# Kernel tuning notes

Hardware: AMD Instinct MI355X
Metric: run time of the kernel (lower is better)

The kernel has to match this reference:

```python
import jax, jax.numpy as jnp
import numpy as np

DRN = 0.4
TWO_PI = 2.0 * np.pi


def _mlp(x, ws, bs):
    # torch_geometric MLP with act='LeakyRelu' (slope 0.01), dropout=0 (eval), norm treated as identity (eval running stats)
    for w, b in zip(ws[:-1], bs[:-1]):
        x = jax.nn.leaky_relu(x @ w + b, 0.01)
    return x @ ws[-1] + bs[-1]


def _conv(x, ws, bs):
    # x: [B, N, F] = [pt, h..., ang_re, ang_im]. Dense masked equivalent of radius-graph EdgeConv.
    ang = x[..., -2:]
    d2 = jnp.sum((ang[:, :, None, :] - ang[:, None, :, :]) ** 2, -1)
    adj = (d2 <= DRN * DRN).astype(x.dtype)  # [B,N,N], i=target, j=source, self-loops included (radius ball)
    h = x[..., 1:-2]
    B, N, H = h.shape
    hi = jnp.broadcast_to(h[:, :, None, :], (B, N, N, H))
    hj = jnp.broadcast_to(h[:, None, :, :], (B, N, N, H))
    re, im = ang[..., 0], ang[..., 1]
    r2 = re * re + im * im
    nrm = jnp.maximum(jnp.sqrt(r2[:, :, None] * r2[:, None, :]), 1e-12)
    cos = (re[:, :, None] * re[:, None, :] + im[:, :, None] * im[:, None, :]) / nrm
    sin = (im[:, :, None] * re[:, None, :] - re[:, :, None] * im[:, None, :]) / nrm
    feat = jnp.concatenate([hi, hj, hj - hi, cos[..., None], sin[..., None]], -1)
    m = _mlp(feat, ws, bs)  # [B,N,N,H_out+1]
    # pt-weighted aggregation: message pt is the TARGET's pt (x_i[:, :1] in torch code)
    pt = x[..., 0]
    msg_pt = pt[:, :, None] * adj
    denom = jnp.sum(msg_pt, -1, keepdims=True)
    w = jnp.where(denom > 0, msg_pt / denom, 0.0)  # nan_to_num equivalent
    agg = jnp.einsum('bij,bijk->bik', w, m)
    sw = jnp.sum(w, -1)
    agg_pt = pt * sw                      # sum_j w * pt_i
    agg_ang = ang * sw[..., None]          # sum_j w * ang_i
    # phase renormalization: exp(2*pi*i*gamma) * (re + i*im)
    gamma = agg[..., -1]
    c, s = jnp.cos(TWO_PI * gamma), jnp.sin(TWO_PI * gamma)
    re2 = c * agg_ang[..., 0] - s * agg_ang[..., 1]
    im2 = s * agg_ang[..., 0] + c * agg_ang[..., 1]
    return jnp.concatenate([agg_pt[..., None], agg[..., :-1], re2[..., None], im2[..., None]], -1)


def _forward(pt, angles, c0w, c0b, c1w, c1b, rw, rb):
    absz = jnp.sqrt(jnp.sum(angles ** 2, -1))  # |view_as_complex(angles)|
    x = jnp.concatenate([pt[..., None], absz[..., None], angles], -1)
    x = _conv(x, c0w, c0b)
    x = _conv(x, c1w, c1b)
    # pt-weighted readout over particles
    ptf = x[..., 0]
    denom = jnp.sum(ptf, -1, keepdims=True)
    wj = jnp.where(denom > 0, ptf / denom, 0.0)
    xg = jnp.einsum('bn,bnf->bf', wj, x[..., 1:])
    logits = _mlp(xg[:, :-2], rw, rb)
    return jnp.concatenate([jax.nn.sigmoid(logits), xg[:, -2:]], -1)


def setup_inputs() -> dict:
    key = jax.random.key(0)
    ks = jax.random.split(key, 16)
    B, N = 128, 128
    pt = jax.random.uniform(ks[0], (B, N), jnp.float32, 0.05, 1.0)  # all > 0 so mask is all-true
    angles = 0.25 * jax.random.normal(ks[1], (B, N, 2), jnp.float32)

    def lin(k, i, o):
        return (0.2 / np.sqrt(i)) * jax.random.normal(k, (i, o), jnp.float32) * np.sqrt(i)

    H = 16
    return {
        'pt': pt, 'angles': angles,
        'c0_w0': lin(ks[2], 5, H), 'c0_b0': jnp.zeros((H,), jnp.float32),
        'c0_w1': lin(ks[3], H, H + 1), 'c0_b1': jnp.zeros((H + 1,), jnp.float32),
        'c1_w0': lin(ks[4], 3 * H + 2, H), 'c1_b0': jnp.zeros((H,), jnp.float32),
        'c1_w1': lin(ks[5], H, H + 1), 'c1_b1': jnp.zeros((H + 1,), jnp.float32),
        'r_w0': lin(ks[6], H, 32), 'r_b0': jnp.zeros((32,), jnp.float32),
        'r_w1': lin(ks[7], 32, 32), 'r_b1': jnp.zeros((32,), jnp.float32),
        'r_w2': lin(ks[8], 32, 1), 'r_b2': jnp.zeros((1,), jnp.float32),
    }


def reference(pt, angles, c0_w0, c0_b0, c0_w1, c0_b1, c1_w0, c1_b0, c1_w1, c1_b1, r_w0, r_b0, r_w1, r_b1, r_w2, r_b2):
    return _forward(pt, angles, (c0_w0, c0_w1), (c0_b0, c0_b1), (c1_w0, c1_w1), (c1_b0, c1_b1), (r_w0, r_w1, r_w2), (r_b0, r_b1, r_b2))
```

## Files before the change

### kernel.cpp

```cpp
#include <hip/hip_runtime.h>
#include <math.h>


#define BB 128
#define NN 128
#define BN (BB * NN)
#define TWO_PI_F 6.283185307179586f

template <int CTRL>
__device__ __forceinline__ float dpp_add(float x) {
    int t = __builtin_amdgcn_update_dpp(0, __float_as_int(x), CTRL, 0xF, 0xF, true);
    return x + __int_as_float(t);
}

__device__ __forceinline__ float wave_sum64(float x) {
    x = dpp_add<0xB1>(x);
    x = dpp_add<0x4E>(x);
    x = dpp_add<0x114>(x);
    x = dpp_add<0x118>(x);
    x = dpp_add<0x142>(x);
    x = dpp_add<0x143>(x);
    return __int_as_float(__builtin_amdgcn_readlane(__float_as_int(x), 63));
}

template <int L>
__global__ __launch_bounds__(256) void conv_kernel(
    const float* __restrict__ ang,
    const float* __restrict__ u,
    const float* __restrict__ v,
    const float* __restrict__ w0,
    const float* __restrict__ b0,
    const float* __restrict__ w1,
    const float* __restrict__ b1,
    const float* __restrict__ nw0,
    const float* __restrict__ nb0,
    float* __restrict__ out_u,
    float* __restrict__ out_v,
    float* __restrict__ out_ang,
    float* __restrict__ y)
{
    const int lane = threadIdx.x & 63;
    const int wid  = threadIdx.x >> 6;
    const int ni   = __builtin_amdgcn_readfirstlane(blockIdx.x * 4 + wid);
    const int base = ni & ~(NN - 1);

    const float rei = ang[2 * ni], imi = ang[2 * ni + 1];
    const float r2i = rei * rei + imi * imi;

    constexpr int cosrow = (L == 0) ? 3 : 48;

    float u0b[16];
    float q0[16];
    if constexpr (L == 0) {
        float abszi = __builtin_amdgcn_sqrtf(r2i);
        #pragma unroll
        for (int k = 0; k < 16; ++k) {
            u0b[k] = fmaf(abszi, w0[k] - w0[32 + k], b0[k]);
            q0[k]  = w0[16 + k] + w0[32 + k];
        }
    } else {
        #pragma unroll
        for (int k = 0; k < 16; ++k) u0b[k] = u[ni * 16 + k];
    }

    float A[16];
    #pragma unroll
    for (int k = 0; k < 16; ++k) A[k] = 0.0f;
    int deg = 0;

    #pragma unroll
    for (int jj = 0; jj < 2; ++jj) {
        const int nj = base + lane + jj * 64;
        const float rej = ang[2 * nj], imj = ang[2 * nj + 1];

        const float dre = rei - rej, dim = imi - imj;
        const float d2 = dre * dre + dim * dim;
        const bool isadj = (d2 <= 0.16f);
        deg += (int)__popcll(__ballot(isadj));
        const float adjf = isadj ? 1.0f : 0.0f;

        const float r2j = rej * rej + imj * imj;
        const float inv = fminf(rsqrtf(r2i * r2j), 1e12f);
        const float cosv = fmaf(rei, rej, imi * imj) * inv;
        const float sinv = fmaf(imi, rej, -(rei * imj)) * inv;

        float abszj = 0.0f;
        float vj[16];
        if constexpr (L == 0) {
            abszj = __builtin_amdgcn_sqrtf(r2j);
        } else {
            const float4* vp = (const float4*)(v + (size_t)nj * 16);
            float4 a0 = vp[0], a1 = vp[1], a2 = vp[2], a3 = vp[3];
            vj[0] = a0.x; vj[1] = a0.y; vj[2]  = a0.z; vj[3]  = a0.w;
            vj[4] = a1.x; vj[5] = a1.y; vj[6]  = a1.z; vj[7]  = a1.w;
            vj[8] = a2.x; vj[9] = a2.y; vj[10] = a2.z; vj[11] = a2.w;
            vj[12] = a3.x; vj[13] = a3.y; vj[14] = a3.z; vj[15] = a3.w;
        }

        #pragma unroll
        for (int k = 0; k < 16; ++k) {
            float z;
            if constexpr (L == 0) z = fmaf(abszj, q0[k], u0b[k]);
            else                  z = u0b[k] + vj[k];
            z = fmaf(cosv, w0[cosrow * 16 + k], z);
            z = fmaf(sinv, w0[(cosrow + 1) * 16 + k], z);
            float a = fmaxf(z, 0.01f * z);
            A[k] = fmaf(a, adjf, A[k]);
        }
    }

    float Ak[16];
    #pragma unroll
    for (int k = 0; k < 16; ++k) Ak[k] = wave_sum64(A[k]);
    const float invdeg = 1.0f / (float)deg;

    float aggv = 0.0f;
    if (lane < 17) {
        float s = 0.0f;
        #pragma unroll
        for (int k = 0; k < 16; ++k) s = fmaf(Ak[k], w1[k * 17 + lane], s);
        aggv = fmaf(s, invdeg, b1[lane]);
    }

    __shared__ float h1s[4][16];

    if constexpr (L == 0) {
        if (lane < 16) h1s[wid][lane] = aggv;
        if (lane == 16) {
            float th = TWO_PI_F * aggv;
            float cs = cosf(th), sn = sinf(th);
            out_ang[2 * ni]     = cs * rei - sn * imi;
            out_ang[2 * ni + 1] = sn * rei + cs * imi;
        }
        __syncthreads();
        if (lane < 32) {
            const int k = lane & 15;
            const bool isU = lane < 16;
            const int off = isU ? 0 : 256;
            const float sgn = isU ? -1.0f : 1.0f;
            float acc = isU ? nb0[k] : 0.0f;
            #pragma unroll
            for (int c = 0; c < 16; ++c) {
                float wa  = nw0[off + c * 16 + k];
                float wcv = nw0[512 + c * 16 + k];
                acc = fmaf(h1s[wid][c], fmaf(sgn, wcv, wa), acc);
            }
            if (isU) out_u[ni * 16 + k] = acc;
            else     out_v[ni * 16 + k] = acc;
        }
    } else {
        if (lane < 16) y[ni * 18 + lane] = aggv;
        if (lane == 16) {
            float th = TWO_PI_F * aggv;
            float cs = cosf(th), sn = sinf(th);
            y[ni * 18 + 16] = cs * rei - sn * imi;
            y[ni * 18 + 17] = sn * rei + cs * imi;
        }
    }
}

__global__ __launch_bounds__(128) void readout_kernel(
    const float* __restrict__ pt,
    const float* __restrict__ y,
    const float* __restrict__ w0, const float* __restrict__ b0,
    const float* __restrict__ w1, const float* __restrict__ b1,
    const float* __restrict__ w2, const float* __restrict__ b2,
    float* __restrict__ out) {
    int b = blockIdx.x;
    int tid = threadIdx.x;
    int n = b * NN + tid;
    float ptf = pt[n];
    const float* yn = y + (size_t)n * 18;

    __shared__ float sred[2][18];
    __shared__ float xg[18];
    __shared__ float h1s[32];

    float tot = ptf;
#pragma unroll
    for (int off = 32; off; off >>= 1) tot += __shfl_xor(tot, off);
    if ((tid & 63) == 0) sred[tid >> 6][0] = tot;
    __syncthreads();
    float denom = sred[0][0] + sred[1][0];
    float wj = (denom > 0.0f) ? (ptf / denom) : 0.0f;
    __syncthreads();

    float vals[18];
#pragma unroll
    for (int f = 0; f < 18; ++f) vals[f] = wj * yn[f];
#pragma unroll
    for (int f = 0; f < 18; ++f) {
        float s = vals[f];
#pragma unroll
        for (int off = 32; off; off >>= 1) s += __shfl_xor(s, off);
        vals[f] = s;
    }
    if ((tid & 63) == 0) {
#pragma unroll
        for (int f = 0; f < 18; ++f) sred[tid >> 6][f] = vals[f];
    }
    __syncthreads();
    if (tid < 18) xg[tid] = sred[0][tid] + sred[1][tid];
    __syncthreads();

    if (tid < 32) {
        float h = b0[tid];
#pragma unroll
        for (int k = 0; k < 16; ++k) h = fmaf(xg[k], w0[k * 32 + tid], h);
        h = (h >= 0.0f) ? h : 0.01f * h;
        h1s[tid] = h;
    }
    __syncthreads();
    if (tid < 32) {
        float h = b1[tid];
#pragma unroll
        for (int k = 0; k < 32; ++k) h = fmaf(h1s[k], w1[k * 32 + tid], h);
        h = (h >= 0.0f) ? h : 0.01f * h;
        float p = h * w2[tid];
#pragma unroll
        for (int off = 16; off; off >>= 1) p += __shfl_xor(p, off, 32);
        if (tid == 0) {
            float logit = p + b2[0];
            out[b * 3 + 0] = 1.0f / (1.0f + expf(-logit));
            out[b * 3 + 1] = xg[16];
            out[b * 3 + 2] = xg[17];
        }
    }
}

extern "C" void kernel_launch(void* const* d_in, const int* in_sizes, int n_in,
                              void* d_out, int out_size, void* d_ws, size_t ws_size,
                              hipStream_t stream) {
    const float* pt    = (const float*)d_in[0];
    const float* ang   = (const float*)d_in[1];
    const float* c0_w0 = (const float*)d_in[2];
    const float* c0_b0 = (const float*)d_in[3];
    const float* c0_w1 = (const float*)d_in[4];
    const float* c0_b1 = (const float*)d_in[5];
    const float* c1_w0 = (const float*)d_in[6];
    const float* c1_b0 = (const float*)d_in[7];
    const float* c1_w1 = (const float*)d_in[8];
    const float* c1_b1 = (const float*)d_in[9];
    const float* r_w0  = (const float*)d_in[10];
    const float* r_b0  = (const float*)d_in[11];
    const float* r_w1  = (const float*)d_in[12];
    const float* r_b1  = (const float*)d_in[13];
    const float* r_w2  = (const float*)d_in[14];
    const float* r_b2  = (const float*)d_in[15];
    float* out = (float*)d_out;
    float* ws = (float*)d_ws;

    float* u1b  = ws;
    float* v1   = u1b + (size_t)BN * 16;
    float* ang1 = v1 + (size_t)BN * 16;
    float* y1   = ang1 + (size_t)BN * 2;

    hipLaunchKernelGGL((conv_kernel<0>), dim3(BN / 4), dim3(256), 0, stream,
                       ang, (const float*)nullptr, (const float*)nullptr,
                       c0_w0, c0_b0, c0_w1, c0_b1,
                       c1_w0, c1_b0, u1b, v1, ang1, (float*)nullptr);
    hipLaunchKernelGGL((conv_kernel<1>), dim3(BN / 4), dim3(256), 0, stream,
                       ang1, u1b, v1,
                       c1_w0, (const float*)nullptr, c1_w1, c1_b1,
                       (const float*)nullptr, (const float*)nullptr,
                       (float*)nullptr, (float*)nullptr, (float*)nullptr, y1);
    hipLaunchKernelGGL(readout_kernel, dim3(BB), dim3(128), 0, stream,
                       pt, y1, r_w0, r_b0, r_w1, r_b1, r_w2, r_b2, out);
}
```

Before: 37.12 us.

## Remap conv kernels to one lane per target node and fuse readout pooling

Each lane now owns one target node, and the 128 source nodes are split across the four waves of a block. Source angles and features are staged once in LDS, and per-wave partial sums are combined through shared memory. This replaces the earlier design of one wave per target node with 16 cross-lane DPP reductions per node, and cuts the grid from 4096 blocks to 256. The pt-weighted pooling moves into conv1 as per-block partial sums, so the y buffer disappears and the readout kernel shrinks to a tiny MLP. In exchange the grid has only 256 blocks of four waves, so occupancy is low and the per-lane serial work is longer; the 1e12 clamp on the inverse norm is also dropped.

```diff
diff --git a/kernel.cpp b/kernel.cpp
--- a/kernel.cpp
+++ b/kernel.cpp
@@ -5,7 +5,6 @@
 #define BB 128
 #define NN 128
 #define BN (BB * NN)
-#define TWO_PI_F 6.283185307179586f
 
 template <int CTRL>
 __device__ __forceinline__ float dpp_add(float x) {
@@ -23,205 +22,304 @@
     return __int_as_float(__builtin_amdgcn_readlane(__float_as_int(x), 63));
 }
 
-template <int L>
-__global__ __launch_bounds__(256) void conv_kernel(
+__global__ __launch_bounds__(256) void conv0_kernel(
     const float* __restrict__ ang,
-    const float* __restrict__ u,
-    const float* __restrict__ v,
     const float* __restrict__ w0,
     const float* __restrict__ b0,
     const float* __restrict__ w1,
     const float* __restrict__ b1,
     const float* __restrict__ nw0,
     const float* __restrict__ nb0,
-    float* __restrict__ out_u,
-    float* __restrict__ out_v,
-    float* __restrict__ out_ang,
-    float* __restrict__ y)
+    float* __restrict__ ang1,
+    float* __restrict__ u1,
+    float* __restrict__ v1)
 {
-    const int lane = threadIdx.x & 63;
-    const int wid  = threadIdx.x >> 6;
-    const int ni   = __builtin_amdgcn_readfirstlane(blockIdx.x * 4 + wid);
-    const int base = ni & ~(NN - 1);
-
-    const float rei = ang[2 * ni], imi = ang[2 * ni + 1];
-    const float r2i = rei * rei + imi * imi;
-
-    constexpr int cosrow = (L == 0) ? 3 : 48;
-
-    float u0b[16];
-    float q0[16];
-    if constexpr (L == 0) {
-        float abszi = __builtin_amdgcn_sqrtf(r2i);
+    const int tid  = threadIdx.x;
+    const int lane = tid & 63;
+    const int wid  = tid >> 6;
+    const int b     = blockIdx.x >> 1;
+    const int ihalf = blockIdx.x & 1;
+    const int nodebase = b * NN;
+    const int ni = nodebase + ihalf * 64 + lane;
+
+    __shared__ float4 jdat[NN];
+    __shared__ float Ap[4][17][64];
+
+    if (tid < NN) {
+        float2 a = ((const float2*)ang)[nodebase + tid];
+        float r2 = a.x * a.x + a.y * a.y;
+        float absz = __builtin_amdgcn_sqrtf(r2);
+        float inv = __builtin_amdgcn_rsqf(r2);
+        jdat[tid] = make_float4(a.x, a.y, absz, inv);
+    }
+    __syncthreads();
+
+    const float4 my = jdat[ihalf * 64 + lane];
+    const float rei = my.x, imi = my.y, abszi = my.z, invi = my.w;
+
+    float u0b[16], q0[16];
+    #pragma unroll
+    for (int k = 0; k < 16; ++k) {
+        u0b[k] = fmaf(abszi, w0[k] - w0[32 + k], b0[k]);
+        q0[k]  = w0[16 + k] + w0[32 + k];
+    }
+
+    float A[16];
+    #pragma unroll
+    for (int k = 0; k < 16; ++k) A[k] = 0.0f;
+    float degf = 0.0f;
+
+    const int jbase = wid * 32;
+    float4 cd = jdat[jbase];
+    #pragma unroll 2
+    for (int jj = 0; jj < 32; ++jj) {
+        float4 nd = jdat[jbase + ((jj + 1) & 31)];
+        const float rej = cd.x, imj = cd.y, abszj = cd.z, invj = cd.w;
+        float dre = rei - rej, dim = imi - imj;
+        float d2 = fmaf(dre, dre, dim * dim);
+        float adjf = (d2 <= 0.16f) ? 1.0f : 0.0f;
+        degf += adjf;
+        float inv = invi * invj;
+        float cosv = fmaf(rei, rej, imi * imj) * inv;
+        float sinv = fmaf(imi, rej, -(rei * imj)) * inv;
         #pragma unroll
         for (int k = 0; k < 16; ++k) {
-            u0b[k] = fmaf(abszi, w0[k] - w0[32 + k], b0[k]);
-            q0[k]  = w0[16 + k] + w0[32 + k];
-        }
-    } else {
-        #pragma unroll
-        for (int k = 0; k < 16; ++k) u0b[k] = u[ni * 16 + k];
-    }
-
-    float A[16];
-    #pragma unroll
-    for (int k = 0; k < 16; ++k) A[k] = 0.0f;
-    int deg = 0;
-
-    #pragma unroll
-    for (int jj = 0; jj < 2; ++jj) {
-        const int nj = base + lane + jj * 64;
-        const float rej = ang[2 * nj], imj = ang[2 * nj + 1];
-
-        const float dre = rei - rej, dim = imi - imj;
-        const float d2 = dre * dre + dim * dim;
-        const bool isadj = (d2 <= 0.16f);
-        deg += (int)__popcll(__ballot(isadj));
-        const float adjf = isadj ? 1.0f : 0.0f;
-
-        const float r2j = rej * rej + imj * imj;
-        const float inv = fminf(rsqrtf(r2i * r2j), 1e12f);
-        const float cosv = fmaf(rei, rej, imi * imj) * inv;
-        const float sinv = fmaf(imi, rej, -(rei * imj)) * inv;
-
-        float abszj = 0.0f;
-        float vj[16];
-        if constexpr (L == 0) {
-            abszj = __builtin_amdgcn_sqrtf(r2j);
-        } else {
-            const float4* vp = (const float4*)(v + (size_t)nj * 16);
-            float4 a0 = vp[0], a1 = vp[1], a2 = vp[2], a3 = vp[3];
-            vj[0] = a0.x; vj[1] = a0.y; vj[2]  = a0.z; vj[3]  = a0.w;
-            vj[4] = a1.x; vj[5] = a1.y; vj[6]  = a1.z; vj[7]  = a1.w;
-            vj[8] = a2.x; vj[9] = a2.y; vj[10] = a2.z; vj[11] = a2.w;
-            vj[12] = a3.x; vj[13] = a3.y; vj[14] = a3.z; vj[15] = a3.w;
-        }
-
-        #pragma unroll
-        for (int k = 0; k < 16; ++k) {
-            float z;
-            if constexpr (L == 0) z = fmaf(abszj, q0[k], u0b[k]);
-            else                  z = u0b[k] + vj[k];
-            z = fmaf(cosv, w0[cosrow * 16 + k], z);
-            z = fmaf(sinv, w0[(cosrow + 1) * 16 + k], z);
+            float z = fmaf(abszj, q0[k], u0b[k]);
+            z = fmaf(cosv, w0[48 + k], z);
+            z = fmaf(sinv, w0[64 + k], z);
             float a = fmaxf(z, 0.01f * z);
             A[k] = fmaf(a, adjf, A[k]);
         }
-    }
-
-    float Ak[16];
-    #pragma unroll
-    for (int k = 0; k < 16; ++k) Ak[k] = wave_sum64(A[k]);
-    const float invdeg = 1.0f / (float)deg;
-
-    float aggv = 0.0f;
-    if (lane < 17) {
+        cd = nd;
+    }
+
+    #pragma unroll
+    for (int k = 0; k < 16; ++k) Ap[wid][k][lane] = A[k];
+    Ap[wid][16][lane] = degf;
+    __syncthreads();
+    #pragma unroll
+    for (int w2 = 0; w2 < 4; ++w2) {
+        if (w2 == wid) continue;
+        #pragma unroll
+        for (int k = 0; k < 16; ++k) A[k] += Ap[w2][k][lane];
+        degf += Ap[w2][16][lane];
+    }
+
+    const float invdeg = __builtin_amdgcn_rcpf(degf);
+    float m[17];
+    #pragma unroll
+    for (int t = 0; t < 17; ++t) {
         float s = 0.0f;
         #pragma unroll
-        for (int k = 0; k < 16; ++k) s = fmaf(Ak[k], w1[k * 17 + lane], s);
-        aggv = fmaf(s, invdeg, b1[lane]);
-    }
-
-    __shared__ float h1s[4][16];
-
-    if constexpr (L == 0) {
-        if (lane < 16) h1s[wid][lane] = aggv;
-        if (lane == 16) {
-            float th = TWO_PI_F * aggv;
-            float cs = cosf(th), sn = sinf(th);
-            out_ang[2 * ni]     = cs * rei - sn * imi;
-            out_ang[2 * ni + 1] = sn * rei + cs * imi;
-        }
-        __syncthreads();
-        if (lane < 32) {
-            const int k = lane & 15;
-            const bool isU = lane < 16;
-            const int off = isU ? 0 : 256;
-            const float sgn = isU ? -1.0f : 1.0f;
-            float acc = isU ? nb0[k] : 0.0f;
+        for (int k = 0; k < 16; ++k) s = fmaf(A[k], w1[k * 17 + t], s);
+        m[t] = fmaf(s, invdeg, b1[t]);
+    }
+
+    if (wid == 0) {
+        float g = m[16] - floorf(m[16]);
+        float cs = __builtin_amdgcn_cosf(g);
+        float sn = __builtin_amdgcn_sinf(g);
+        float re2 = cs * rei - sn * imi;
+        float im2 = fmaf(sn, rei, cs * imi);
+        ((float2*)ang1)[ni] = make_float2(re2, im2);
+    }
+
+    const int isV = wid >> 1;
+    const int khalf = wid & 1;
+    float acc[8];
+    if (isV == 0) {
+        #pragma unroll
+        for (int kk = 0; kk < 8; ++kk) {
+            const int kp = khalf * 8 + kk;
+            float a = nb0[kp];
             #pragma unroll
             for (int c = 0; c < 16; ++c) {
-                float wa  = nw0[off + c * 16 + k];
-                float wcv = nw0[512 + c * 16 + k];
-                acc = fmaf(h1s[wid][c], fmaf(sgn, wcv, wa), acc);
+                a = fmaf(m[c], nw0[c * 16 + kp], a);
+                a = fmaf(-m[c], nw0[512 + c * 16 + kp], a);
             }
-            if (isU) out_u[ni * 16 + k] = acc;
-            else     out_v[ni * 16 + k] = acc;
-        }
+            acc[kk] = a;
+        }
+        float4* up = (float4*)(u1 + (size_t)ni * 16);
+        up[khalf * 2 + 0] = make_float4(acc[0], acc[1], acc[2], acc[3]);
+        up[khalf * 2 + 1] = make_float4(acc[4], acc[5], acc[6], acc[7]);
     } else {
-        if (lane < 16) y[ni * 18 + lane] = aggv;
-        if (lane == 16) {
-            float th = TWO_PI_F * aggv;
-            float cs = cosf(th), sn = sinf(th);
-            y[ni * 18 + 16] = cs * rei - sn * imi;
-            y[ni * 18 + 17] = sn * rei + cs * imi;
-        }
-    }
-}
-
-__global__ __launch_bounds__(128) void readout_kernel(
+        #pragma unroll
+        for (int kk = 0; kk < 8; ++kk) {
+            const int kp = khalf * 8 + kk;
+            float a = 0.0f;
+            #pragma unroll
+            for (int c = 0; c < 16; ++c) {
+                a = fmaf(m[c], nw0[256 + c * 16 + kp], a);
+                a = fmaf(m[c], nw0[512 + c * 16 + kp], a);
+            }
+            acc[kk] = a;
+        }
+        float4* vp = (float4*)(v1 + (size_t)ni * 16);
+        vp[khalf * 2 + 0] = make_float4(acc[0], acc[1], acc[2], acc[3]);
+        vp[khalf * 2 + 1] = make_float4(acc[4], acc[5], acc[6], acc[7]);
+    }
+}
+
+__global__ __launch_bounds__(256) void conv1_kernel(
     const float* __restrict__ pt,
-    const float* __restrict__ y,
+    const float* __restrict__ ang1,
+    const float* __restrict__ u1,
+    const float* __restrict__ v1,
+    const float* __restrict__ w0,
+    const float* __restrict__ w1,
+    const float* __restrict__ b1,
+    float* __restrict__ part)
+{
+    const int tid  = threadIdx.x;
+    const int lane = tid & 63;
+    const int wid  = tid >> 6;
+    const int b     = blockIdx.x >> 1;
+    const int ihalf = blockIdx.x & 1;
+    const int nodebase = b * NN;
+    const int ni = nodebase + ihalf * 64 + lane;
+
+    __shared__ float4 jdat[NN];
+    __shared__ float4 jv[NN][4];
+    __shared__ float Ap[4][17][64];
+
+    if (tid < NN) {
+        float2 a = ((const float2*)ang1)[nodebase + tid];
+        float r2 = a.x * a.x + a.y * a.y;
+        float inv = __builtin_amdgcn_rsqf(r2);
+        jdat[tid] = make_float4(a.x, a.y, inv, 0.0f);
+        const float4* vg = (const float4*)(v1 + (size_t)(nodebase + tid) * 16);
+        jv[tid][0] = vg[0]; jv[tid][1] = vg[1];
+        jv[tid][2] = vg[2]; jv[tid][3] = vg[3];
+    }
+
+    float u0b[16];
+    {
+        const float4* ug = (const float4*)(u1 + (size_t)ni * 16);
+        float4 a0 = ug[0], a1 = ug[1], a2 = ug[2], a3 = ug[3];
+        u0b[0] = a0.x; u0b[1] = a0.y; u0b[2]  = a0.z; u0b[3]  = a0.w;
+        u0b[4] = a1.x; u0b[5] = a1.y; u0b[6]  = a1.z; u0b[7]  = a1.w;
+        u0b[8] = a2.x; u0b[9] = a2.y; u0b[10] = a2.z; u0b[11] = a2.w;
+        u0b[12] = a3.x; u0b[13] = a3.y; u0b[14] = a3.z; u0b[15] = a3.w;
+    }
+    float ptf = 0.0f;
+    if (wid == 0) ptf = pt[ni];
+    __syncthreads();
+
+    const float4 my = jdat[ihalf * 64 + lane];
+    const float rei = my.x, imi = my.y, invi = my.z;
+
+    float A[16];
+    #pragma unroll
+    for (int k = 0; k < 16; ++k) A[k] = 0.0f;
+    float degf = 0.0f;
+
+    const int jbase = wid * 32;
+    float4 cd = jdat[jbase];
+    float4 c0 = jv[jbase][0], c1 = jv[jbase][1], c2 = jv[jbase][2], c3 = jv[jbase][3];
+    #pragma unroll 2
+    for (int jj = 0; jj < 32; ++jj) {
+        const int nj = jbase + ((jj + 1) & 31);
+        float4 nd = jdat[nj];
+        float4 n0 = jv[nj][0], n1 = jv[nj][1], n2 = jv[nj][2], n3 = jv[nj][3];
+        const float rej = cd.x, imj = cd.y, invj = cd.z;
+        float dre = rei - rej, dim = imi - imj;
+        float d2 = fmaf(dre, dre, dim * dim);
+        float adjf = (d2 <= 0.16f) ? 1.0f : 0.0f;
+        degf += adjf;
+        float inv = invi * invj;
+        float cosv = fmaf(rei, rej, imi * imj) * inv;
+        float sinv = fmaf(imi, rej, -(rei * imj)) * inv;
+        const float vj[16] = {c0.x, c0.y, c0.z, c0.w, c1.x, c1.y, c1.z, c1.w,
+                              c2.x, c2.y, c2.z, c2.w, c3.x, c3.y, c3.z, c3.w};
+        #pragma unroll
+        for (int k = 0; k < 16; ++k) {
+            float z = u0b[k] + vj[k];
+            z = fmaf(cosv, w0[768 + k], z);
+            z = fmaf(sinv, w0[784 + k], z);
+            float a = fmaxf(z, 0.01f * z);
+            A[k] = fmaf(a, adjf, A[k]);
+        }
+        cd = nd; c0 = n0; c1 = n1; c2 = n2; c3 = n3;
+    }
+
+    #pragma unroll
+    for (int k = 0; k < 16; ++k) Ap[wid][k][lane] = A[k];
+    Ap[wid][16][lane] = degf;
+    __syncthreads();
+
+    if (wid == 0) {
+        #pragma unroll
+        for (int w2 = 1; w2 < 4; ++w2) {
+            #pragma unroll
+            for (int k = 0; k < 16; ++k) A[k] += Ap[w2][k][lane];
+            degf += Ap[w2][16][lane];
+        }
+        const float invdeg = __builtin_amdgcn_rcpf(degf);
+        float m[17];
+        #pragma unroll
+        for (int t = 0; t < 17; ++t) {
+            float s = 0.0f;
+            #pragma unroll
+            for (int k = 0; k < 16; ++k) s = fmaf(A[k], w1[k * 17 + t], s);
+            m[t] = fmaf(s, invdeg, b1[t]);
+        }
+        float g = m[16] - floorf(m[16]);
+        float cs = __builtin_amdgcn_cosf(g);
+        float sn = __builtin_amdgcn_sinf(g);
+        float re2 = cs * rei - sn * imi;
+        float im2 = fmaf(sn, rei, cs * imi);
+
+        float* pout = part + (size_t)blockIdx.x * 20;
+        float s0 = wave_sum64(ptf);
+        if (lane == 0) pout[0] = s0;
+        #pragma unroll
+        for (int f = 0; f < 16; ++f) {
+            float sf = wave_sum64(ptf * m[f]);
+            if (lane == 0) pout[1 + f] = sf;
+        }
+        float sre = wave_sum64(ptf * re2);
+        float sim = wave_sum64(ptf * im2);
+        if (lane == 0) { pout[17] = sre; pout[18] = sim; }
+    }
+}
+
+__global__ __launch_bounds__(64) void readout_kernel(
+    const float* __restrict__ part,
     const float* __restrict__ w0, const float* __restrict__ b0,
     const float* __restrict__ w1, const float* __restrict__ b1,
     const float* __restrict__ w2, const float* __restrict__ b2,
     float* __restrict__ out) {
-    int b = blockIdx.x;
-    int tid = threadIdx.x;
-    int n = b * NN + tid;
-    float ptf = pt[n];
-    const float* yn = y + (size_t)n * 18;
-
-    __shared__ float sred[2][18];
+    const int b = blockIdx.x;
+    const int t = threadIdx.x;
+    const float* p0 = part + (size_t)(2 * b) * 20;
+    const float* p1 = p0 + 20;
+
     __shared__ float xg[18];
     __shared__ float h1s[32];
 
-    float tot = ptf;
-#pragma unroll
-    for (int off = 32; off; off >>= 1) tot += __shfl_xor(tot, off);
-    if ((tid & 63) == 0) sred[tid >> 6][0] = tot;
-    __syncthreads();
-    float denom = sred[0][0] + sred[1][0];
-    float wj = (denom > 0.0f) ? (ptf / denom) : 0.0f;
-    __syncthreads();
-
-    float vals[18];
-#pragma unroll
-    for (int f = 0; f < 18; ++f) vals[f] = wj * yn[f];
-#pragma unroll
-    for (int f = 0; f < 18; ++f) {
-        float s = vals[f];
-#pragma unroll
-        for (int off = 32; off; off >>= 1) s += __shfl_xor(s, off);
-        vals[f] = s;
-    }
-    if ((tid & 63) == 0) {
-#pragma unroll
-        for (int f = 0; f < 18; ++f) sred[tid >> 6][f] = vals[f];
-    }
-    __syncthreads();
-    if (tid < 18) xg[tid] = sred[0][tid] + sred[1][tid];
-    __syncthreads();
-
-    if (tid < 32) {
-        float h = b0[tid];
-#pragma unroll
-        for (int k = 0; k < 16; ++k) h = fmaf(xg[k], w0[k * 32 + tid], h);
-        h = (h >= 0.0f) ? h : 0.01f * h;
-        h1s[tid] = h;
-    }
-    __syncthreads();
-    if (tid < 32) {
-        float h = b1[tid];
-#pragma unroll
-        for (int k = 0; k < 32; ++k) h = fmaf(h1s[k], w1[k * 32 + tid], h);
-        h = (h >= 0.0f) ? h : 0.01f * h;
-        float p = h * w2[tid];
-#pragma unroll
+    float denom = p0[0] + p1[0];
+    float invd = (denom > 0.0f) ? __builtin_amdgcn_rcpf(denom) : 0.0f;
+    if (t < 18) xg[t] = (p0[1 + t] + p1[1 + t]) * invd;
+    __syncthreads();
+
+    if (t < 32) {
+        float h = b0[t];
+        #pragma unroll
+        for (int k = 0; k < 16; ++k) h = fmaf(xg[k], w0[k * 32 + t], h);
+        h = fmaxf(h, 0.01f * h);
+        h1s[t] = h;
+    }
+    __syncthreads();
+    if (t < 32) {
+        float h = b1[t];
+        #pragma unroll
+        for (int k = 0; k < 32; ++k) h = fmaf(h1s[k], w1[k * 32 + t], h);
+        h = fmaxf(h, 0.01f * h);
+        float p = h * w2[t];
+        #pragma unroll
         for (int off = 16; off; off >>= 1) p += __shfl_xor(p, off, 32);
-        if (tid == 0) {
-            float logit = p + b2[0];
-            out[b * 3 + 0] = 1.0f / (1.0f + expf(-logit));
+        if (t == 0) {
+            out[b * 3 + 0] = 1.0f / (1.0f + expf(-(p + b2[0])));
             out[b * 3 + 1] = xg[16];
             out[b * 3 + 2] = xg[17];
         }
@@ -250,20 +348,16 @@
     float* out = (float*)d_out;
     float* ws = (float*)d_ws;
 
-    float* u1b  = ws;
-    float* v1   = u1b + (size_t)BN * 16;
-    float* ang1 = v1 + (size_t)BN * 16;
-    float* y1   = ang1 + (size_t)BN * 2;
-
-    hipLaunchKernelGGL((conv_kernel<0>), dim3(BN / 4), dim3(256), 0, stream,
-                       ang, (const float*)nullptr, (const float*)nullptr,
-                       c0_w0, c0_b0, c0_w1, c0_b1,
-                       c1_w0, c1_b0, u1b, v1, ang1, (float*)nullptr);
-    hipLaunchKernelGGL((conv_kernel<1>), dim3(BN / 4), dim3(256), 0, stream,
-                       ang1, u1b, v1,
-                       c1_w0, (const float*)nullptr, c1_w1, c1_b1,
-                       (const float*)nullptr, (const float*)nullptr,
-                       (float*)nullptr, (float*)nullptr, (float*)nullptr, y1);
-    hipLaunchKernelGGL(readout_kernel, dim3(BB), dim3(128), 0, stream,
-                       pt, y1, r_w0, r_b0, r_w1, r_b1, r_w2, r_b2, out);
-}
+    float* ang1 = ws;
+    float* u1   = ang1 + (size_t)BN * 2;
+    float* v1   = u1 + (size_t)BN * 16;
+    float* partb = v1 + (size_t)BN * 16;
+
+    hipLaunchKernelGGL(conv0_kernel, dim3(256), dim3(256), 0, stream,
+                       ang, c0_w0, c0_b0, c0_w1, c0_b1, c1_w0, c1_b0,
+                       ang1, u1, v1);
+    hipLaunchKernelGGL(conv1_kernel, dim3(256), dim3(256), 0, stream,
+                       pt, ang1, u1, v1, c1_w0, c1_w1, c1_b1, partb);
+    hipLaunchKernelGGL(readout_kernel, dim3(BB), dim3(64), 0, stream,
+                       partb, r_w0, r_b0, r_w1, r_b1, r_w2, r_b2, out);
+}
```

Result: slower. 42.08 us (+13.4%).
